# Kernel optimization log

Hardware: AMD Instinct MI355X
Metric: run time of the kernel (lower is better)

## Reference

```python
import jax, jax.numpy as jnp
import numpy as np

B, T, DK, DV = 64, 2048, 128, 128
INIT_SCALE = 0.01


def setup_inputs() -> dict:
    key = jax.random.key(0)
    ks = jax.random.split(key, 7)
    return {
        "query": jax.random.normal(ks[0], (B, T, DK), dtype=jnp.float32),
        "key": jax.random.normal(ks[1], (B, T, DK), dtype=jnp.float32),
        "value": jax.random.normal(ks[2], (B, T, DV), dtype=jnp.float32),
        "alpha": jax.random.uniform(ks[3], (B, T, 1), dtype=jnp.float32),
        "rho": jax.random.uniform(ks[4], (B, T, 1), dtype=jnp.float32),
        "lam": jax.random.uniform(ks[5], (B, T, 1), dtype=jnp.float32),
        "init_state": jax.random.normal(ks[6], (B, DK, DV), dtype=jnp.float32) * INIT_SCALE,
    }


def reference(query, key, value, alpha, rho, lam, init_state):
    """Decayed outer-product fast-weight memory, scanned over time.

    Per step t:  M_t = lam_t * M_{t-1} + (rho_t * alpha_t) * (k_t outer v_t)
                 r_t = q_t^T M_t                      # [B, D_v]
    Returns readouts [B, T, D_v].
    """
    # time-major inputs for scan: [T, B, ...]
    tm = lambda x: jnp.swapaxes(x, 0, 1)
    xs = (tm(query), tm(key), tm(value), tm(alpha), tm(rho), tm(lam))

    def step(M, inp):
        q, k, v, a, r, l = inp  # q,k: [B,DK]; v: [B,DV]; a,r,l: [B,1]
        write_scale = (r * a)[:, :, None]          # [B,1,1]
        outer = k[:, :, None] * v[:, None, :]      # [B,DK,DV]
        M = l[:, :, None] * M + write_scale * outer
        read = jnp.einsum('bk,bkv->bv', q, M)      # [B,DV]
        return M, read

    _, reads = jax.lax.scan(step, init_state, xs)
    return jnp.swapaxes(reads, 0, 1)  # [B,T,DV]
```

## Files before the change

kernel.cpp:

```cpp
#include <hip/hip_runtime.h>
#include <hip/hip_bf16.h>


typedef float  f32x4  __attribute__((ext_vector_type(4)));
typedef short  bf16x8 __attribute__((ext_vector_type(8)));

constexpr int B_ = 64, T_ = 2048;
constexpr int NSPLIT = 4;
constexpr int CT = 64;
constexpr int NCH = T_ / CT;

__device__ __forceinline__ bf16x8 cvt8(float4 a, float4 b) {
  union { __hip_bfloat162 h2[4]; bf16x8 v; } u;
  u.h2[0] = __float22bfloat162_rn(make_float2(a.x, a.y));
  u.h2[1] = __float22bfloat162_rn(make_float2(a.z, a.w));
  u.h2[2] = __float22bfloat162_rn(make_float2(b.x, b.y));
  u.h2[3] = __float22bfloat162_rn(make_float2(b.z, b.w));
  return u.v;
}

__device__ __forceinline__ float fexp2(float x) { return __builtin_exp2f(x); }
__device__ __forceinline__ float flog2(float x) { return __builtin_log2f(x); }

#define MFMA(a, b, c) __builtin_amdgcn_mfma_f32_16x16x32_bf16((a), (b), (c), 0, 0, 0)

__device__ __forceinline__ void gload16(const float* gsrc, float* ldst) {
  __builtin_amdgcn_global_load_lds(
      (const __attribute__((address_space(1))) void*)gsrc,
      (__attribute__((address_space(3))) void*)ldst, 16, 0, 0);
}

__global__ __launch_bounds__(256, 1) void lmm_ct64p(
    const float* __restrict__ q_g, const float* __restrict__ k_g,
    const float* __restrict__ v_g, const float* __restrict__ a_g,
    const float* __restrict__ r_g, const float* __restrict__ l_g,
    const float* __restrict__ m0_g, float* __restrict__ out_g)
{
  const int bid   = blockIdx.y * NSPLIT + blockIdx.x;
  const int b     = (bid & 7) * 8 + (bid >> 5);
  const int split = (bid >> 3) & 3;

  const int tid   = threadIdx.x;
  const int w     = tid >> 6;
  const int lane  = tid & 63;
  const int m     = lane & 15;
  const int quad  = lane >> 4;
  const int jbase = split * 32;

  __shared__ __align__(16) float klds[2][64][128];
  __shared__ __align__(16) __hip_bfloat16 MhT [32][136];
  __shared__ __align__(16) __hip_bfloat16 VwT [32][72];
  __shared__ __align__(16) __hip_bfloat16 VwTd[32][72];
  __shared__ __align__(16) __hip_bfloat16 Sd[4][16][72];

  const float* qb = q_g + (size_t)b * T_ * 128;
  const float* kb = k_g + (size_t)b * T_ * 128;
  const float* vb = v_g + (size_t)b * T_ * 128;
  const float* ab = a_g + (size_t)b * T_;
  const float* rb = r_g + (size_t)b * T_;
  const float* lb = l_g + (size_t)b * T_;
  float*       ob = out_g + (size_t)b * T_ * 128;

  f32x4 M[2][2];
  #pragma unroll
  for (int it = 0; it < 2; ++it)
    #pragma unroll
    for (int jt = 0; jt < 2; ++jt)
      #pragma unroll
      for (int r = 0; r < 4; ++r)
        M[it][jt][r] =
            m0_g[((size_t)b * 128 + w * 32 + it * 16 + quad * 4 + r) * 128 +
                 jbase + jt * 16 + m];

  const int jv   = tid & 31;
  const int s8   = tid >> 5;
  const int prow = lane >> 5;
  const int pblk = lane & 31;

  float4 qpre[4][2];
  float  vpre[8];
  float  lpre, apre, rpre;

  lpre = lb[lane]; apre = ab[lane]; rpre = rb[lane];
  #pragma unroll
  for (int c = 0; c < 8; ++c) {
    const int row = w * 16 + c * 2 + prow;
    gload16(kb + (size_t)row * 128 + ((pblk ^ (row & 7)) << 2),
            &klds[0][w * 16 + c * 2][0]);
  }
  #pragma unroll
  for (int ks = 0; ks < 4; ++ks) {
    const float* p = qb + (size_t)(w * 16 + m) * 128 + ks * 32 + quad * 8;
    qpre[ks][0] = *(const float4*)p;
    qpre[ks][1] = *(const float4*)(p + 4);
  }
  #pragma unroll
  for (int rep = 0; rep < 8; ++rep)
    vpre[rep] = vb[(size_t)(s8 * 8 + rep) * 128 + jbase + jv];

  #pragma unroll 2
  for (int ch = 0; ch < NCH; ++ch) {
    const int t0   = ch * CT;
    const int tn   = (ch + 1 < NCH) ? t0 + CT : t0;
    const int buf  = ch & 1;
    const int nbuf = buf ^ 1;

    __syncthreads();

    float x = flog2(fmaxf(lpre, 1e-20f));
    #pragma unroll
    for (int d = 1; d < 64; d <<= 1) {
      const float o = __shfl_up(x, d, 64);
      if (lane >= d) x += o;
    }
    const float L2    = x;
    const float L2end = __shfl(L2, 63, 64);
    const float arp   = apre * rpre;

    bf16x8 qf[4];
    #pragma unroll
    for (int ks = 0; ks < 4; ++ks) qf[ks] = cvt8(qpre[ks][0], qpre[ks][1]);

    f32x4 S[4] = {{0.f,0.f,0.f,0.f},{0.f,0.f,0.f,0.f},
                  {0.f,0.f,0.f,0.f},{0.f,0.f,0.f,0.f}};
    #pragma unroll
    for (int sb = 0; sb < 4; ++sb) {
      const int rowk = sb * 16 + m;
      const int xk   = rowk & 7;
      #pragma unroll
      for (int ks = 0; ks < 4; ++ks) {
        const int bk0 = ks * 8 + quad * 2;
        const float4 kA = *(const float4*)&klds[buf][rowk][((bk0      ^ xk) << 2)];
        const float4 kB = *(const float4*)&klds[buf][rowk][(((bk0 + 1) ^ xk) << 2)];
        S[sb] = MFMA(qf[ks], cvt8(kA, kB), S[sb]);
      }
    }

    const int tl0 = w * 16 + quad * 4;
    float tl[4];
    #pragma unroll
    for (int r = 0; r < 4; ++r) tl[r] = __shfl(L2, tl0 + r, 64);
    #pragma unroll
    for (int sb = 0; sb < 4; ++sb) {
      const int   sl_i = sb * 16 + m;
      const float sl   = __shfl(L2, sl_i, 64);
      #pragma unroll
      for (int r = 0; r < 4; ++r) {
        const float dv = (sl_i <= tl0 + r) ? S[sb][r] * fexp2(tl[r] - sl) : 0.f;
        Sd[w][quad * 4 + r][sl_i] = __float2bfloat16(dv);
      }
    }

    {
      float fw[8], fd[8];
      #pragma unroll
      for (int rep = 0; rep < 8; ++rep) {
        const int   s   = s8 * 8 + rep;
        const float arf = __shfl(arp, s, 64);
        const float dcf = fexp2(L2end - __shfl(L2, s, 64));
        fw[rep] = vpre[rep] * arf;
        fd[rep] = fw[rep] * dcf;
      }
      union { __hip_bfloat162 h2[4]; bf16x8 v; } uw, ud;
      #pragma unroll
      for (int p2 = 0; p2 < 4; ++p2) {
        uw.h2[p2] = __float22bfloat162_rn(make_float2(fw[2*p2], fw[2*p2+1]));
        ud.h2[p2] = __float22bfloat162_rn(make_float2(fd[2*p2], fd[2*p2+1]));
      }
      *(bf16x8*)&VwT [jv][s8 * 8] = uw.v;
      *(bf16x8*)&VwTd[jv][s8 * 8] = ud.v;
    }

    #pragma unroll
    for (int it = 0; it < 2; ++it)
      #pragma unroll
      for (int jt = 0; jt < 2; ++jt) {
        union { __hip_bfloat162 h2[2]; uint2 u; } pk;
        pk.h2[0] = __float22bfloat162_rn(make_float2(M[it][jt][0], M[it][jt][1]));
        pk.h2[1] = __float22bfloat162_rn(make_float2(M[it][jt][2], M[it][jt][3]));
        *(uint2*)&MhT[jt * 16 + m][w * 32 + it * 16 + quad * 4] = pk.u;
      }

    __syncthreads();

    lpre = lb[tn + lane]; apre = ab[tn + lane]; rpre = rb[tn + lane];
    #pragma unroll
    for (int c = 0; c < 8; ++c) {
      const int row = w * 16 + c * 2 + prow;
      gload16(kb + (size_t)(tn + row) * 128 + ((pblk ^ (row & 7)) << 2),
              &klds[nbuf][w * 16 + c * 2][0]);
    }
    #pragma unroll
    for (int ks = 0; ks < 4; ++ks) {
      const float* p = qb + (size_t)(tn + w * 16 + m) * 128 + ks * 32 + quad * 8;
      qpre[ks][0] = *(const float4*)p;
      qpre[ks][1] = *(const float4*)(p + 4);
    }
    #pragma unroll
    for (int rep = 0; rep < 8; ++rep)
      vpre[rep] = vb[(size_t)(tn + s8 * 8 + rep) * 128 + jbase + jv];

    f32x4 R[2] = {{0.f,0.f,0.f,0.f},{0.f,0.f,0.f,0.f}};
    #pragma unroll
    for (int ks = 0; ks < 4; ++ks)
      #pragma unroll
      for (int jt = 0; jt < 2; ++jt) {
        const bf16x8 mb = *(const bf16x8*)&MhT[jt * 16 + m][ks * 32 + quad * 8];
        R[jt] = MFMA(qf[ks], mb, R[jt]);
      }
    #pragma unroll
    for (int r = 0; r < 4; ++r) {
      const float et = fexp2(tl[r]);
      R[0][r] *= et; R[1][r] *= et;
    }
    #pragma unroll
    for (int kk = 0; kk < 2; ++kk) {
      const bf16x8 sa = *(const bf16x8*)&Sd[w][m][kk * 32 + quad * 8];
      #pragma unroll
      for (int jt = 0; jt < 2; ++jt) {
        const bf16x8 vw = *(const bf16x8*)&VwT[jt * 16 + m][kk * 32 + quad * 8];
        R[jt] = MFMA(sa, vw, R[jt]);
      }
    }
    #pragma unroll
    for (int jt = 0; jt < 2; ++jt)
      #pragma unroll
      for (int r = 0; r < 4; ++r)
        ob[(size_t)(t0 + w * 16 + quad * 4 + r) * 128 + jbase + jt * 16 + m] =
            R[jt][r];

    const float eend = fexp2(L2end);
    #pragma unroll
    for (int it = 0; it < 2; ++it)
      #pragma unroll
      for (int jt = 0; jt < 2; ++jt)
        #pragma unroll
        for (int r = 0; r < 4; ++r) M[it][jt][r] *= eend;
    #pragma unroll
    for (int kk = 0; kk < 2; ++kk)
      #pragma unroll
      for (int it = 0; it < 2; ++it) {
        float kv[8];
        #pragma unroll
        for (int u = 0; u < 8; ++u) {
          const int rows = kk * 32 + quad * 8 + u;
          const int col  = w * 32 + it * 16 + m;
          kv[u] = klds[buf][rows][(((col >> 2) ^ (rows & 7)) << 2) | (col & 3)];
        }
        const bf16x8 af = cvt8(make_float4(kv[0], kv[1], kv[2], kv[3]),
                               make_float4(kv[4], kv[5], kv[6], kv[7]));
        #pragma unroll
        for (int jt = 0; jt < 2; ++jt) {
          const bf16x8 vd = *(const bf16x8*)&VwTd[jt * 16 + m][kk * 32 + quad * 8];
          M[it][jt] = MFMA(af, vd, M[it][jt]);
        }
      }
  }
}

extern "C" void kernel_launch(void* const* d_in, const int* in_sizes, int n_in,
                              void* d_out, int out_size, void* d_ws, size_t ws_size,
                              hipStream_t stream) {
  const float* q  = (const float*)d_in[0];
  const float* k  = (const float*)d_in[1];
  const float* v  = (const float*)d_in[2];
  const float* a  = (const float*)d_in[3];
  const float* r  = (const float*)d_in[4];
  const float* l  = (const float*)d_in[5];
  const float* m0 = (const float*)d_in[6];
  float* out = (float*)d_out;

  dim3 grid(NSPLIT, B_);
  lmm_ct64p<<<grid, 256, 0, stream>>>(q, k, v, a, r, l, m0, out);
}
```

Baseline: 311.3 us.

## Split chunk work across eight waves and move next-chunk prefetch earlier

Doubles the workgroup from 4 to 8 waves and halves each wave's share. Each wave now owns 16 rows of the state slice, one 16x16 readout tile and half of the intra-chunk score block, with wave pairs sharing a query tile. Prefetch of the next chunk's K, Q, V and decay inputs moves to right after the first barrier so loads overlap more compute, and the LDS swizzle for K gains an extra XOR term to reduce bank conflicts. The aim is more latency hiding per CU, at the cost of more threads per barrier and some duplicated L2 scan and query conversion work.

```diff
diff --git a/kernel.cpp b/kernel.cpp
--- a/kernel.cpp
+++ b/kernel.cpp
@@ -4,6 +4,7 @@
 
 typedef float  f32x4  __attribute__((ext_vector_type(4)));
 typedef short  bf16x8 __attribute__((ext_vector_type(8)));
+typedef short  bf16x4 __attribute__((ext_vector_type(4)));
 
 constexpr int B_ = 64, T_ = 2048;
 constexpr int NSPLIT = 4;
@@ -22,6 +23,10 @@
 __device__ __forceinline__ float fexp2(float x) { return __builtin_exp2f(x); }
 __device__ __forceinline__ float flog2(float x) { return __builtin_log2f(x); }
 
+__device__ __forceinline__ int xk_of(int row) {
+  return (row & 7) ^ (((row >> 3) & 3) << 3);
+}
+
 #define MFMA(a, b, c) __builtin_amdgcn_mfma_f32_16x16x32_bf16((a), (b), (c), 0, 0, 0)
 
 __device__ __forceinline__ void gload16(const float* gsrc, float* ldst) {
@@ -30,7 +35,7 @@
       (__attribute__((address_space(3))) void*)ldst, 16, 0, 0);
 }
 
-__global__ __launch_bounds__(256, 1) void lmm_ct64p(
+__global__ __launch_bounds__(512, 1) void lmm_w8(
     const float* __restrict__ q_g, const float* __restrict__ k_g,
     const float* __restrict__ v_g, const float* __restrict__ a_g,
     const float* __restrict__ r_g, const float* __restrict__ l_g,
@@ -45,6 +50,8 @@
   const int lane  = tid & 63;
   const int m     = lane & 15;
   const int quad  = lane >> 4;
+  const int tw    = w >> 1;
+  const int half  = w & 1;
   const int jbase = split * 32;
 
   __shared__ __align__(16) float klds[2][64][128];
@@ -61,16 +68,13 @@
   const float* lb = l_g + (size_t)b * T_;
   float*       ob = out_g + (size_t)b * T_ * 128;
 
-  f32x4 M[2][2];
-  #pragma unroll
-  for (int it = 0; it < 2; ++it)
-    #pragma unroll
-    for (int jt = 0; jt < 2; ++jt)
-      #pragma unroll
-      for (int r = 0; r < 4; ++r)
-        M[it][jt][r] =
-            m0_g[((size_t)b * 128 + w * 32 + it * 16 + quad * 4 + r) * 128 +
-                 jbase + jt * 16 + m];
+  f32x4 M[2];
+  #pragma unroll
+  for (int jt = 0; jt < 2; ++jt)
+    #pragma unroll
+    for (int r = 0; r < 4; ++r)
+      M[jt][r] = m0_g[((size_t)b * 128 + w * 16 + quad * 4 + r) * 128 +
+                      jbase + jt * 16 + m];
 
   const int jv   = tid & 31;
   const int s8   = tid >> 5;
@@ -78,25 +82,25 @@
   const int pblk = lane & 31;
 
   float4 qpre[4][2];
-  float  vpre[8];
+  float  vpre[4];
   float  lpre, apre, rpre;
 
   lpre = lb[lane]; apre = ab[lane]; rpre = rb[lane];
   #pragma unroll
-  for (int c = 0; c < 8; ++c) {
-    const int row = w * 16 + c * 2 + prow;
-    gload16(kb + (size_t)row * 128 + ((pblk ^ (row & 7)) << 2),
-            &klds[0][w * 16 + c * 2][0]);
+  for (int c = 0; c < 4; ++c) {
+    const int row = w * 8 + c * 2 + prow;
+    gload16(kb + (size_t)row * 128 + ((pblk ^ xk_of(row)) << 2),
+            &klds[0][w * 8 + c * 2][0]);
   }
   #pragma unroll
   for (int ks = 0; ks < 4; ++ks) {
-    const float* p = qb + (size_t)(w * 16 + m) * 128 + ks * 32 + quad * 8;
+    const float* p = qb + (size_t)(tw * 16 + m) * 128 + ks * 32 + quad * 8;
     qpre[ks][0] = *(const float4*)p;
     qpre[ks][1] = *(const float4*)(p + 4);
   }
   #pragma unroll
-  for (int rep = 0; rep < 8; ++rep)
-    vpre[rep] = vb[(size_t)(s8 * 8 + rep) * 128 + jbase + jv];
+  for (int rep = 0; rep < 4; ++rep)
+    vpre[rep] = vb[(size_t)(s8 * 4 + rep) * 128 + jbase + jv];
 
   #pragma unroll 2
   for (int ch = 0; ch < NCH; ++ch) {
@@ -107,6 +111,13 @@
 
     __syncthreads();
 
+    #pragma unroll
+    for (int c = 0; c < 4; ++c) {
+      const int row = w * 8 + c * 2 + prow;
+      gload16(kb + (size_t)(tn + row) * 128 + ((pblk ^ xk_of(row)) << 2),
+              &klds[nbuf][w * 8 + c * 2][0]);
+    }
+
     float x = flog2(fmaxf(lpre, 1e-20f));
     #pragma unroll
     for (int d = 1; d < 64; d <<= 1) {
@@ -121,12 +132,37 @@
     #pragma unroll
     for (int ks = 0; ks < 4; ++ks) qf[ks] = cvt8(qpre[ks][0], qpre[ks][1]);
 
-    f32x4 S[4] = {{0.f,0.f,0.f,0.f},{0.f,0.f,0.f,0.f},
-                  {0.f,0.f,0.f,0.f},{0.f,0.f,0.f,0.f}};
-    #pragma unroll
-    for (int sb = 0; sb < 4; ++sb) {
-      const int rowk = sb * 16 + m;
-      const int xk   = rowk & 7;
+    const int tl0 = tw * 16 + quad * 4;
+    float tl[4];
+    #pragma unroll
+    for (int r = 0; r < 4; ++r) tl[r] = __shfl(L2, tl0 + r, 64);
+
+    float fw[4], fd[4];
+    #pragma unroll
+    for (int rep = 0; rep < 4; ++rep) {
+      const int   s   = s8 * 4 + rep;
+      const float arf = __shfl(arp, s, 64);
+      const float dcf = fexp2(L2end - __shfl(L2, s, 64));
+      fw[rep] = vpre[rep] * arf;
+      fd[rep] = fw[rep] * dcf;
+    }
+
+    lpre = lb[tn + lane]; apre = ab[tn + lane]; rpre = rb[tn + lane];
+    #pragma unroll
+    for (int ks = 0; ks < 4; ++ks) {
+      const float* p = qb + (size_t)(tn + tw * 16 + m) * 128 + ks * 32 + quad * 8;
+      qpre[ks][0] = *(const float4*)p;
+      qpre[ks][1] = *(const float4*)(p + 4);
+    }
+    #pragma unroll
+    for (int rep = 0; rep < 4; ++rep)
+      vpre[rep] = vb[(size_t)(tn + s8 * 4 + rep) * 128 + jbase + jv];
+
+    f32x4 S[2] = {{0.f,0.f,0.f,0.f},{0.f,0.f,0.f,0.f}};
+    #pragma unroll
+    for (int sb = 0; sb < 2; ++sb) {
+      const int rowk = half * 32 + sb * 16 + m;
+      const int xk   = xk_of(rowk);
       #pragma unroll
       for (int ks = 0; ks < 4; ++ks) {
         const int bk0 = ks * 8 + quad * 2;
@@ -136,125 +172,79 @@
       }
     }
 
-    const int tl0 = w * 16 + quad * 4;
-    float tl[4];
-    #pragma unroll
-    for (int r = 0; r < 4; ++r) tl[r] = __shfl(L2, tl0 + r, 64);
-    #pragma unroll
-    for (int sb = 0; sb < 4; ++sb) {
-      const int   sl_i = sb * 16 + m;
+    #pragma unroll
+    for (int sb = 0; sb < 2; ++sb) {
+      const int   sl_i = half * 32 + sb * 16 + m;
       const float sl   = __shfl(L2, sl_i, 64);
       #pragma unroll
       for (int r = 0; r < 4; ++r) {
         const float dv = (sl_i <= tl0 + r) ? S[sb][r] * fexp2(tl[r] - sl) : 0.f;
-        Sd[w][quad * 4 + r][sl_i] = __float2bfloat16(dv);
+        Sd[tw][quad * 4 + r][sl_i] = __float2bfloat16(dv);
       }
     }
 
     {
-      float fw[8], fd[8];
-      #pragma unroll
-      for (int rep = 0; rep < 8; ++rep) {
-        const int   s   = s8 * 8 + rep;
-        const float arf = __shfl(arp, s, 64);
-        const float dcf = fexp2(L2end - __shfl(L2, s, 64));
-        fw[rep] = vpre[rep] * arf;
-        fd[rep] = fw[rep] * dcf;
-      }
-      union { __hip_bfloat162 h2[4]; bf16x8 v; } uw, ud;
-      #pragma unroll
-      for (int p2 = 0; p2 < 4; ++p2) {
-        uw.h2[p2] = __float22bfloat162_rn(make_float2(fw[2*p2], fw[2*p2+1]));
-        ud.h2[p2] = __float22bfloat162_rn(make_float2(fd[2*p2], fd[2*p2+1]));
-      }
-      *(bf16x8*)&VwT [jv][s8 * 8] = uw.v;
-      *(bf16x8*)&VwTd[jv][s8 * 8] = ud.v;
-    }
-
-    #pragma unroll
-    for (int it = 0; it < 2; ++it)
+      union { __hip_bfloat162 h2[2]; bf16x4 v; } uw, ud;
+      uw.h2[0] = __float22bfloat162_rn(make_float2(fw[0], fw[1]));
+      uw.h2[1] = __float22bfloat162_rn(make_float2(fw[2], fw[3]));
+      ud.h2[0] = __float22bfloat162_rn(make_float2(fd[0], fd[1]));
+      ud.h2[1] = __float22bfloat162_rn(make_float2(fd[2], fd[3]));
+      *(bf16x4*)&VwT [jv][s8 * 4] = uw.v;
+      *(bf16x4*)&VwTd[jv][s8 * 4] = ud.v;
+    }
+
+    #pragma unroll
+    for (int jt = 0; jt < 2; ++jt) {
+      union { __hip_bfloat162 h2[2]; uint2 u; } pk;
+      pk.h2[0] = __float22bfloat162_rn(make_float2(M[jt][0], M[jt][1]));
+      pk.h2[1] = __float22bfloat162_rn(make_float2(M[jt][2], M[jt][3]));
+      *(uint2*)&MhT[jt * 16 + m][w * 16 + quad * 4] = pk.u;
+    }
+
+    __syncthreads();
+
+    f32x4 R = {0.f, 0.f, 0.f, 0.f};
+    #pragma unroll
+    for (int ks = 0; ks < 4; ++ks) {
+      const bf16x8 mb = *(const bf16x8*)&MhT[half * 16 + m][ks * 32 + quad * 8];
+      R = MFMA(qf[ks], mb, R);
+    }
+    #pragma unroll
+    for (int r = 0; r < 4; ++r) R[r] *= fexp2(tl[r]);
+
+    #pragma unroll
+    for (int kk = 0; kk < 2; ++kk) {
+      const bf16x8 sa = *(const bf16x8*)&Sd[tw][m][kk * 32 + quad * 8];
+      const bf16x8 vw = *(const bf16x8*)&VwT[half * 16 + m][kk * 32 + quad * 8];
+      R = MFMA(sa, vw, R);
+    }
+    #pragma unroll
+    for (int r = 0; r < 4; ++r)
+      ob[(size_t)(t0 + tw * 16 + quad * 4 + r) * 128 + jbase + half * 16 + m] =
+          R[r];
+
+    const float eend = fexp2(L2end);
+    #pragma unroll
+    for (int jt = 0; jt < 2; ++jt)
+      #pragma unroll
+      for (int r = 0; r < 4; ++r) M[jt][r] *= eend;
+    #pragma unroll
+    for (int kk = 0; kk < 2; ++kk) {
+      float kv[8];
+      #pragma unroll
+      for (int u = 0; u < 8; ++u) {
+        const int rows = kk * 32 + quad * 8 + u;
+        const int col  = w * 16 + m;
+        kv[u] = klds[buf][rows][(((col >> 2) ^ xk_of(rows)) << 2) | (col & 3)];
+      }
+      const bf16x8 af = cvt8(make_float4(kv[0], kv[1], kv[2], kv[3]),
+                             make_float4(kv[4], kv[5], kv[6], kv[7]));
       #pragma unroll
       for (int jt = 0; jt < 2; ++jt) {
-        union { __hip_bfloat162 h2[2]; uint2 u; } pk;
-        pk.h2[0] = __float22bfloat162_rn(make_float2(M[it][jt][0], M[it][jt][1]));
-        pk.h2[1] = __float22bfloat162_rn(make_float2(M[it][jt][2], M[it][jt][3]));
-        *(uint2*)&MhT[jt * 16 + m][w * 32 + it * 16 + quad * 4] = pk.u;
-      }
-
-    __syncthreads();
-
-    lpre = lb[tn + lane]; apre = ab[tn + lane]; rpre = rb[tn + lane];
-    #pragma unroll
-    for (int c = 0; c < 8; ++c) {
-      const int row = w * 16 + c * 2 + prow;
-      gload16(kb + (size_t)(tn + row) * 128 + ((pblk ^ (row & 7)) << 2),
-              &klds[nbuf][w * 16 + c * 2][0]);
-    }
-    #pragma unroll
-    for (int ks = 0; ks < 4; ++ks) {
-      const float* p = qb + (size_t)(tn + w * 16 + m) * 128 + ks * 32 + quad * 8;
-      qpre[ks][0] = *(const float4*)p;
-      qpre[ks][1] = *(const float4*)(p + 4);
-    }
-    #pragma unroll
-    for (int rep = 0; rep < 8; ++rep)
-      vpre[rep] = vb[(size_t)(tn + s8 * 8 + rep) * 128 + jbase + jv];
-
-    f32x4 R[2] = {{0.f,0.f,0.f,0.f},{0.f,0.f,0.f,0.f}};
-    #pragma unroll
-    for (int ks = 0; ks < 4; ++ks)
-      #pragma unroll
-      for (int jt = 0; jt < 2; ++jt) {
-        const bf16x8 mb = *(const bf16x8*)&MhT[jt * 16 + m][ks * 32 + quad * 8];
-        R[jt] = MFMA(qf[ks], mb, R[jt]);
-      }
-    #pragma unroll
-    for (int r = 0; r < 4; ++r) {
-      const float et = fexp2(tl[r]);
-      R[0][r] *= et; R[1][r] *= et;
-    }
-    #pragma unroll
-    for (int kk = 0; kk < 2; ++kk) {
-      const bf16x8 sa = *(const bf16x8*)&Sd[w][m][kk * 32 + quad * 8];
-      #pragma unroll
-      for (int jt = 0; jt < 2; ++jt) {
-        const bf16x8 vw = *(const bf16x8*)&VwT[jt * 16 + m][kk * 32 + quad * 8];
-        R[jt] = MFMA(sa, vw, R[jt]);
-      }
-    }
-    #pragma unroll
-    for (int jt = 0; jt < 2; ++jt)
-      #pragma unroll
-      for (int r = 0; r < 4; ++r)
-        ob[(size_t)(t0 + w * 16 + quad * 4 + r) * 128 + jbase + jt * 16 + m] =
-            R[jt][r];
-
-    const float eend = fexp2(L2end);
-    #pragma unroll
-    for (int it = 0; it < 2; ++it)
-      #pragma unroll
-      for (int jt = 0; jt < 2; ++jt)
-        #pragma unroll
-        for (int r = 0; r < 4; ++r) M[it][jt][r] *= eend;
-    #pragma unroll
-    for (int kk = 0; kk < 2; ++kk)
-      #pragma unroll
-      for (int it = 0; it < 2; ++it) {
-        float kv[8];
-        #pragma unroll
-        for (int u = 0; u < 8; ++u) {
-          const int rows = kk * 32 + quad * 8 + u;
-          const int col  = w * 32 + it * 16 + m;
-          kv[u] = klds[buf][rows][(((col >> 2) ^ (rows & 7)) << 2) | (col & 3)];
-        }
-        const bf16x8 af = cvt8(make_float4(kv[0], kv[1], kv[2], kv[3]),
-                               make_float4(kv[4], kv[5], kv[6], kv[7]));
-        #pragma unroll
-        for (int jt = 0; jt < 2; ++jt) {
-          const bf16x8 vd = *(const bf16x8*)&VwTd[jt * 16 + m][kk * 32 + quad * 8];
-          M[it][jt] = MFMA(af, vd, M[it][jt]);
-        }
-      }
+        const bf16x8 vd = *(const bf16x8*)&VwTd[jt * 16 + m][kk * 32 + quad * 8];
+        M[jt] = MFMA(af, vd, M[jt]);
+      }
+    }
   }
 }
 
@@ -271,5 +261,5 @@
   float* out = (float*)d_out;
 
   dim3 grid(NSPLIT, B_);
-  lmm_ct64p<<<grid, 256, 0, stream>>>(q, k, v, a, r, l, m0, out);
-}
+  lmm_w8<<<grid, 512, 0, stream>>>(q, k, v, a, r, l, m0, out);
+}
```

New measurement: 312.8 us. Within noise of the previous version (+0.5%).
